# Performance work log

Hardware: AMD Instinct MI355X
Metric: run time of the kernel (lower is better)

The kernel has to match this reference:

```python
import jax, jax.numpy as jnp
import numpy as np

B, T, C = 4, 4096, 1024
NEG_INF = -1e38


def setup_inputs() -> dict:
    key = jax.random.key(0)
    ks = jax.random.split(key, 5)
    scale = 0.02  # realistic init scale for CxC projections
    x = jax.random.normal(ks[0], (B, T, C), dtype=jnp.float32)
    key_w = jax.random.normal(ks[1], (C, C), dtype=jnp.float32) * scale
    value_w = jax.random.normal(ks[2], (C, C), dtype=jnp.float32) * scale
    receptance_w = jax.random.normal(ks[3], (C, C), dtype=jnp.float32) * scale
    output_w = jax.random.normal(ks[4], (C, C), dtype=jnp.float32) * scale
    # deterministic param init matching the module's __init__
    time_decay = -5.0 + 8.0 * (jnp.arange(C, dtype=jnp.float32) / (C - 1)) ** 0.7
    time_first = jnp.full((C,), -3.0, dtype=jnp.float32)
    # initial WKV state as in forward() when state is None
    aa0 = jnp.zeros((B, C), dtype=jnp.float32)
    bb0 = jnp.zeros((B, C), dtype=jnp.float32)
    pp0 = jnp.full((B, C), NEG_INF, dtype=jnp.float32)
    return dict(x=x, key_w=key_w, value_w=value_w, receptance_w=receptance_w,
                output_w=output_w, time_decay=time_decay, time_first=time_first,
                aa0=aa0, bb0=bb0, pp0=pp0)


def reference(x, key_w, value_w, receptance_w, output_w,
              time_decay, time_first, aa0, bb0, pp0):
    # projections (torch Linear: y = x @ W.T)
    k = jnp.einsum('btc,dc->btd', x, key_w)        # [B,T,C]
    v = jnp.einsum('btc,dc->btd', x, value_w)      # [B,T,C]
    r = jax.nn.sigmoid(jnp.einsum('btc,dc->btd', x, receptance_w))
    w = jnp.exp(time_decay)  # [C]
    u = time_first           # [C]

    def step(carry, kv):
        aa, bb, pp = carry           # each [B,C]
        kt, vt = kv                  # each [B,C]
        # output at this step (numerically stabilized exp weighting)
        ww = u + kt
        p = jnp.maximum(pp, ww)
        e1 = jnp.exp(pp - p)
        e2 = jnp.exp(ww - p)
        wkv = (e1 * aa + e2 * vt) / (e1 * bb + e2)
        # state update
        ww2 = pp - w
        p2 = jnp.maximum(ww2, kt)
        e1b = jnp.exp(ww2 - p2)
        e2b = jnp.exp(kt - p2)
        return (e1b * aa + e2b * vt, e1b * bb + e2b, p2), wkv

    k_t = jnp.swapaxes(k, 0, 1)  # [T,B,C]
    v_t = jnp.swapaxes(v, 0, 1)
    (aa, bb, pp), wkv = jax.lax.scan(step, (aa0, bb0, pp0), (k_t, v_t))
    wkv = jnp.swapaxes(wkv, 0, 1)  # [B,T,C]

    out = jnp.einsum('btc,dc->btd', r * wkv, output_w)
    return out, aa, bb, pp
```

## Files before the change

kernel.cpp:

```cpp
#include <hip/hip_runtime.h>
#include <stdint.h>

#define BDIM 4
#define TDIM 4096
#define CDIM 1024
#define MDIM (BDIM * TDIM)
#define SSEG 64
#define LSEG 64
#define NCH  (BDIM * CDIM)

#define GK   1024
#define GK2  2048
#define NTK  16

typedef __attribute__((ext_vector_type(8))) short bf16x8;
typedef __attribute__((ext_vector_type(4))) float f32x4;

__device__ __forceinline__ unsigned short f2bf(float f) {
    unsigned u = __builtin_bit_cast(unsigned, f);
    u = u + 0x7fffu + ((u >> 16) & 1u);
    return (unsigned short)(u >> 16);
}
__device__ __forceinline__ float bf2f(unsigned short h) {
    unsigned u = ((unsigned)h) << 16;
    return __builtin_bit_cast(float, u);
}

typedef __attribute__((address_space(1))) const unsigned int g_u32;
typedef __attribute__((address_space(3))) unsigned int l_u32;
__device__ __forceinline__ void gload_lds16(const void* g, void* l) {
    __builtin_amdgcn_global_load_lds((g_u32*)g, (l_u32*)l, 16, 0, 0);
}

__global__ void castk(const float* __restrict__ src, unsigned short* __restrict__ dst, int n4) {
    int i = blockIdx.x * blockDim.x + threadIdx.x;
    int stride = gridDim.x * blockDim.x;
    for (int j = i; j < n4; j += stride) {
        float4 f = ((const float4*)src)[j];
        ushort4 o;
        o.x = f2bf(f.x); o.y = f2bf(f.y); o.z = f2bf(f.z); o.w = f2bf(f.w);
        ((ushort4*)dst)[j] = o;
    }
}

__global__ void castw(const float* __restrict__ kw, const float* __restrict__ vw,
                      const float* __restrict__ rw, const float* __restrict__ ow,
                      unsigned short* __restrict__ wf, unsigned short* __restrict__ owb) {
    int i = blockIdx.x * 256 + threadIdx.x;
    int m = i >> 18, j = i & 262143;
    const float* s = (m == 0) ? kw : (m == 1) ? vw : (m == 2) ? rw : ow;
    unsigned short* d = (m < 3) ? (wf + (size_t)m * 1048576) : owb;
    float4 f = ((const float4*)s)[j];
    ushort4 o;
    o.x = f2bf(f.x); o.y = f2bf(f.y); o.z = f2bf(f.z); o.w = f2bf(f.w);
    ((ushort4*)d)[j] = o;
}

template <int MODE, int NT>
__global__ __launch_bounds__(512, 2) void gemm256(
    const unsigned short* __restrict__ A,
    const unsigned short* __restrict__ Bw,
    unsigned short* __restrict__ oK, unsigned short* __restrict__ oV,
    unsigned short* __restrict__ oR, float* __restrict__ oF)
{
    extern __shared__ char sh[];
    char* shA = sh;
    char* shB = sh + 65536;

    const int tid  = threadIdx.x;
    const int wave = tid >> 6;
    const int lane = tid & 63;
    const int wm   = wave >> 2;
    const int wn   = wave & 3;
    const int lrow = lane & 15;
    const int koct = lane >> 4;

    const int kb0 = (koct * 16) ^ ((lrow & 7) << 4);
    const int kb1 = kb0 ^ 64;

    const int sr0  = tid >> 3;
    const int sc0  = ((tid & 7) * 16) ^ ((sr0 & 7) << 4);
    const int sr1  = (512 + tid) >> 3;
    const int sc1  = ((tid & 7) * 16) ^ ((sr1 & 7) << 4);
    const int sd0  = tid * 16;
    const int sd1  = 8192 + tid * 16;

    const int bid = blockIdx.x;
    const int xcd = bid & 7;
    const int idx = bid >> 3;
    const int mt  = xcd * 8 + idx / NT;
    const int nt  = idx % NT;
    const size_t row0 = (size_t)mt * 256;
    const size_t col0 = (size_t)nt * 256;

    const char* gA = (const char*)A  + row0 * GK2;
    const char* gB = (const char*)Bw + col0 * GK2;

    auto stage = [&](int tt, int part) {
        if (tt >= NTK) return;
        int slot = tt & 1;
        int isA  = (part < 2) ? 1 : 0;
        int half = part & 1;
        const char* gbase = (isA ? gA : gB) + (size_t)half * 128 * GK2 + tt * 128;
        char* lbase = (isA ? shA : shB) + (slot * 2 + half) * 16384;
        gload_lds16(gbase + (size_t)sr0 * GK2 + sc0, lbase + sd0);
        gload_lds16(gbase + (size_t)sr1 * GK2 + sc1, lbase + sd1);
    };

    stage(0, 0); stage(0, 1); stage(0, 2); stage(0, 3);
    stage(1, 0); stage(1, 1);
    asm volatile("s_waitcnt vmcnt(4)" ::: "memory");
    __builtin_amdgcn_s_barrier();

    f32x4 acc[8][4] = {};
    bf16x8 af[8][2], bf_[4][2];

    {
        const char* ab = shA + wm * 16384 + lrow * 128;
#pragma unroll
        for (int mi = 0; mi < 4; ++mi) {
            af[mi][0] = *(const bf16x8*)(ab + mi * 2048 + kb0);
            af[mi][1] = *(const bf16x8*)(ab + mi * 2048 + kb1);
        }
    }

    for (int t = 0; t < NTK; ++t) {
        const int slot  = t & 1;
        const char* ab  = shA + (slot * 2 + wm) * 16384 + lrow * 128;
        const char* bb  = shB + (slot * 2 + (wn >> 1)) * 16384 + ((wn & 1) * 64 + lrow) * 128;
        const char* abN = shA + (((t + 1) & 1) * 2 + wm) * 16384 + lrow * 128;

#pragma unroll
        for (int ni = 0; ni < 4; ++ni) {
            bf_[ni][0] = *(const bf16x8*)(bb + ni * 2048 + kb0);
            bf_[ni][1] = *(const bf16x8*)(bb + ni * 2048 + kb1);
        }
        stage(t + 1, 2);
        __builtin_amdgcn_s_barrier();
        __builtin_amdgcn_s_setprio(1);
#pragma unroll
        for (int a = 0; a < 4; ++a)
#pragma unroll
            for (int b = 0; b < 2; ++b)
#pragma unroll
                for (int ks = 0; ks < 2; ++ks)
                    acc[a][b] = __builtin_amdgcn_mfma_f32_16x16x32_bf16(af[a][ks], bf_[b][ks], acc[a][b], 0, 0, 0);
        __builtin_amdgcn_s_setprio(0);
        __builtin_amdgcn_s_barrier();

#pragma unroll
        for (int mi = 4; mi < 8; ++mi) {
            af[mi][0] = *(const bf16x8*)(ab + mi * 2048 + kb0);
            af[mi][1] = *(const bf16x8*)(ab + mi * 2048 + kb1);
        }
        stage(t + 1, 3);
        __builtin_amdgcn_s_barrier();
        __builtin_amdgcn_s_setprio(1);
#pragma unroll
        for (int a = 0; a < 4; ++a)
#pragma unroll
            for (int b = 0; b < 2; ++b)
#pragma unroll
                for (int ks = 0; ks < 2; ++ks)
                    acc[a][2 + b] = __builtin_amdgcn_mfma_f32_16x16x32_bf16(af[a][ks], bf_[2 + b][ks], acc[a][2 + b], 0, 0, 0);
        __builtin_amdgcn_s_setprio(0);
        __builtin_amdgcn_s_barrier();

        stage(t + 2, 0);
        __builtin_amdgcn_s_barrier();
        __builtin_amdgcn_s_setprio(1);
#pragma unroll
        for (int a = 0; a < 4; ++a)
#pragma unroll
            for (int b = 0; b < 2; ++b)
#pragma unroll
                for (int ks = 0; ks < 2; ++ks)
                    acc[4 + a][b] = __builtin_amdgcn_mfma_f32_16x16x32_bf16(af[4 + a][ks], bf_[b][ks], acc[4 + a][b], 0, 0, 0);
        __builtin_amdgcn_s_setprio(0);
        if (t <= 13)      asm volatile("s_waitcnt vmcnt(6)" ::: "memory");
        else if (t == 14) asm volatile("s_waitcnt vmcnt(4)" ::: "memory");
        __builtin_amdgcn_s_barrier();

        stage(t + 2, 1);
        if (t + 1 < NTK) {
#pragma unroll
            for (int mi = 0; mi < 4; ++mi) {
                af[mi][0] = *(const bf16x8*)(abN + mi * 2048 + kb0);
                af[mi][1] = *(const bf16x8*)(abN + mi * 2048 + kb1);
            }
        }
        __builtin_amdgcn_s_barrier();
        __builtin_amdgcn_s_setprio(1);
#pragma unroll
        for (int a = 0; a < 4; ++a)
#pragma unroll
            for (int b = 0; b < 2; ++b)
#pragma unroll
                for (int ks = 0; ks < 2; ++ks)
                    acc[4 + a][2 + b] = __builtin_amdgcn_mfma_f32_16x16x32_bf16(af[4 + a][ks], bf_[2 + b][ks], acc[4 + a][2 + b], 0, 0, 0);
        __builtin_amdgcn_s_setprio(0);
        if (t <= 13)      asm volatile("s_waitcnt vmcnt(4)" ::: "memory");
        else if (t == 14) asm volatile("s_waitcnt vmcnt(0)" ::: "memory");
        __builtin_amdgcn_s_barrier();
    }

    const int crow = (lane >> 4) * 4;
    const int ccol = lane & 15;
    if (MODE == 1) {
#pragma unroll
        for (int mi = 0; mi < 8; ++mi)
#pragma unroll
            for (int ni = 0; ni < 4; ++ni) {
                size_t gr = row0 + wm * 128 + mi * 16 + crow;
                size_t gc = col0 + wn * 64 + ni * 16 + ccol;
#pragma unroll
                for (int j = 0; j < 4; ++j)
                    oF[(gr + j) * 1024 + gc] = acc[mi][ni][j];
            }
    } else {
        const int region = nt >> 2;
        unsigned short* dst = (region == 0) ? oK : ((region == 1) ? oV : oR);
        const size_t cb0 = (size_t)(nt & 3) * 256;
#pragma unroll
        for (int mi = 0; mi < 8; ++mi)
#pragma unroll
            for (int ni = 0; ni < 4; ++ni) {
                size_t gr = row0 + wm * 128 + mi * 16 + crow;
                size_t gc = cb0 + wn * 64 + ni * 16 + ccol;
#pragma unroll
                for (int j = 0; j < 4; ++j) {
                    float val = acc[mi][ni][j];
                    if (region == 2) val = 1.0f / (1.0f + __expf(-val));
                    dst[(gr + j) * 1024 + gc] = f2bf(val);
                }
            }
    }
}

__global__ __launch_bounds__(256) void wkv_phase1(
    const unsigned short* __restrict__ kf, const unsigned short* __restrict__ vf,
    const float* __restrict__ td,
    float* __restrict__ segA, float* __restrict__ segB, float* __restrict__ segP)
{
    const int tid  = blockIdx.x * 256 + threadIdx.x;
    const int lane = tid & 63;
    const int wg   = tid >> 6;
    const int cg   = wg & 63;
    const int s    = wg >> 6;
    const int q    = cg * 64 + lane;
    const int b    = q >> 10;
    const int c    = q & (CDIM - 1);

    const float w = __expf(td[c]);

    float aa = 0.0f, bb = 0.0f, pp = -1e38f;
    size_t idx = (size_t)b * TDIM * CDIM + (size_t)(s * LSEG) * CDIM + c;
#pragma unroll 4
    for (int i = 0; i < LSEG; ++i, idx += CDIM) {
        float kt = bf2f(kf[idx]);
        float vt = bf2f(vf[idx]);
        float ww2 = pp - w;
        float p2  = fmaxf(ww2, kt);
        float e1  = __expf(ww2 - p2);
        float e2  = __expf(kt - p2);
        aa = e1 * aa + e2 * vt;
        bb = e1 * bb + e2;
        pp = p2;
    }
    segA[s * NCH + q] = aa;
    segB[s * NCH + q] = bb;
    segP[s * NCH + q] = pp;
}

__global__ __launch_bounds__(256) void wkv_phase2(
    const float* __restrict__ segA, const float* __restrict__ segB, const float* __restrict__ segP,
    const float* __restrict__ td,
    const float* __restrict__ aa0, const float* __restrict__ bb0, const float* __restrict__ pp0,
    float* __restrict__ preA, float* __restrict__ preB, float* __restrict__ preP,
    float* __restrict__ stout)
{
    const int tid = blockIdx.x * 256 + threadIdx.x;
    const int c = tid & (CDIM - 1);
    const float w  = __expf(td[c]);
    const float Lw = (float)LSEG * w;

    float aa = aa0[tid], bb = bb0[tid], pp = pp0[tid];
    for (int s = 0; s < SSEG; ++s) {
        preA[s * NCH + tid] = aa;
        preB[s * NCH + tid] = bb;
        preP[s * NCH + tid] = pp;
        float al = segA[s * NCH + tid];
        float bl = segB[s * NCH + tid];
        float pl = segP[s * NCH + tid];
        float ppd = pp - Lw;
        float p  = fmaxf(ppd, pl);
        float e1 = __expf(ppd - p);
        float e2 = __expf(pl - p);
        aa = e1 * aa + e2 * al;
        bb = e1 * bb + e2 * bl;
        pp = p;
    }
    stout[tid]           = aa;
    stout[NCH + tid]     = bb;
    stout[2 * NCH + tid] = pp;
}

__global__ __launch_bounds__(256) void wkv_phase3(
    const unsigned short* __restrict__ kf, const unsigned short* __restrict__ vf,
    const unsigned short* __restrict__ rb,
    const float* __restrict__ td, const float* __restrict__ tf,
    const float* __restrict__ preA, const float* __restrict__ preB, const float* __restrict__ preP,
    unsigned short* __restrict__ rwkvb)
{
    const int tid  = blockIdx.x * 256 + threadIdx.x;
    const int lane = tid & 63;
    const int wg   = tid >> 6;
    const int cg   = wg & 63;
    const int s    = wg >> 6;
    const int q    = cg * 64 + lane;
    const int b    = q >> 10;
    const int c    = q & (CDIM - 1);

    const float w = __expf(td[c]);
    const float u = tf[c];

    float aa = preA[s * NCH + q];
    float bb = preB[s * NCH + q];
    float pp = preP[s * NCH + q];

    size_t idx = (size_t)b * TDIM * CDIM + (size_t)(s * LSEG) * CDIM + c;
#pragma unroll 4
    for (int i = 0; i < LSEG; ++i, idx += CDIM) {
        float kt = bf2f(kf[idx]);
        float vt = bf2f(vf[idx]);
        float rt = bf2f(rb[idx]);
        float ww = u + kt;
        float p  = fmaxf(pp, ww);
        float e1 = __expf(pp - p);
        float e2 = __expf(ww - p);
        float wkv = (e1 * aa + e2 * vt) / (e1 * bb + e2);
        rwkvb[idx] = f2bf(rt * wkv);
        float ww2 = pp - w;
        float p2  = fmaxf(ww2, kt);
        float e1b = __expf(ww2 - p2);
        float e2b = __expf(kt - p2);
        aa = e1b * aa + e2b * vt;
        bb = e1b * bb + e2b;
        pp = p2;
    }
}

extern "C" void kernel_launch(void* const* d_in, const int* in_sizes, int n_in,
                              void* d_out, int out_size, void* d_ws, size_t ws_size,
                              hipStream_t stream) {
    const float* x   = (const float*)d_in[0];
    const float* kw  = (const float*)d_in[1];
    const float* vw  = (const float*)d_in[2];
    const float* rw  = (const float*)d_in[3];
    const float* ow  = (const float*)d_in[4];
    const float* td  = (const float*)d_in[5];
    const float* tf  = (const float*)d_in[6];
    const float* aa0 = (const float*)d_in[7];
    const float* bb0 = (const float*)d_in[8];
    const float* pp0 = (const float*)d_in[9];
    float* out = (float*)d_out;

    char* ws = (char*)d_ws;
    unsigned short* wf    = (unsigned short*)(ws);
    unsigned short* owb   = (unsigned short*)(ws + 6291456);
    unsigned short* xb    = (unsigned short*)(ws + 8388608);
    unsigned short* kfb   = (unsigned short*)(ws + 41943040);
    unsigned short* vfb   = (unsigned short*)(ws + 75497472);
    unsigned short* rbb   = (unsigned short*)(ws + 109051904);
    unsigned short* rwkvb = (unsigned short*)(ws + 142606336);
    float* segA = (float*)(ws + 176160768);
    float* segB = (float*)(ws + 177209344);
    float* segP = (float*)(ws + 178257920);
    float* preA = (float*)(ws + 179306496);
    float* preB = (float*)(ws + 180355072);
    float* preP = (float*)(ws + 181403648);

    hipFuncSetAttribute((const void*)(gemm256<0, 12>), hipFuncAttributeMaxDynamicSharedMemorySize, 131072);
    hipFuncSetAttribute((const void*)(gemm256<1, 4>),  hipFuncAttributeMaxDynamicSharedMemorySize, 131072);

    castk<<<2048, 256, 0, stream>>>(x, xb, MDIM * CDIM / 4);
    castw<<<4096, 256, 0, stream>>>(kw, vw, rw, ow, wf, owb);

    gemm256<0, 12><<<768, 512, 131072, stream>>>(xb, wf, kfb, vfb, rbb, nullptr);

    wkv_phase1<<<NCH * SSEG / 256, 256, 0, stream>>>(kfb, vfb, td, segA, segB, segP);
    wkv_phase2<<<NCH / 256, 256, 0, stream>>>(segA, segB, segP, td, aa0, bb0, pp0,
                                              preA, preB, preP, out + (size_t)MDIM * CDIM);
    wkv_phase3<<<NCH * SSEG / 256, 256, 0, stream>>>(kfb, vfb, rbb, td, tf,
                                                     preA, preB, preP, rwkvb);

    gemm256<1, 4><<<256, 512, 131072, stream>>>(rwkvb, owb, nullptr, nullptr, nullptr, out);
}
```

Baseline: 223.0 us.

## Loop each GEMM block over K/V/R projections instead of launching 768 blocks

The fused KVR projection GEMM now launches 256 blocks, and each block loops over the three weight matrices (NP=3) for the same A row-tile. Before, 768 blocks each handled one 256x256 output tile. The intent is to cut the grid to one wave of blocks on 256 CUs, avoiding a partial tail wave, and to improve L2 reuse of the A tile across the three projections. The trade-off is that each block runs three times longer serially, and all A tiles are reloaded from global memory on every pass, so latency hiding across blocks is reduced.

```diff
diff --git a/kernel.cpp b/kernel.cpp
--- a/kernel.cpp
+++ b/kernel.cpp
@@ -56,7 +56,7 @@
     ((ushort4*)d)[j] = o;
 }
 
-template <int MODE, int NT>
+template <int MODE, int NT, int NP>
 __global__ __launch_bounds__(512, 2) void gemm256(
     const unsigned short* __restrict__ A,
     const unsigned short* __restrict__ Bw,
@@ -91,149 +91,152 @@
     const int mt  = xcd * 8 + idx / NT;
     const int nt  = idx % NT;
     const size_t row0 = (size_t)mt * 256;
-    const size_t col0 = (size_t)nt * 256;
-
-    const char* gA = (const char*)A  + row0 * GK2;
-    const char* gB = (const char*)Bw + col0 * GK2;
-
-    auto stage = [&](int tt, int part) {
-        if (tt >= NTK) return;
-        int slot = tt & 1;
-        int isA  = (part < 2) ? 1 : 0;
-        int half = part & 1;
-        const char* gbase = (isA ? gA : gB) + (size_t)half * 128 * GK2 + tt * 128;
-        char* lbase = (isA ? shA : shB) + (slot * 2 + half) * 16384;
-        gload_lds16(gbase + (size_t)sr0 * GK2 + sc0, lbase + sd0);
-        gload_lds16(gbase + (size_t)sr1 * GK2 + sc1, lbase + sd1);
-    };
-
-    stage(0, 0); stage(0, 1); stage(0, 2); stage(0, 3);
-    stage(1, 0); stage(1, 1);
-    asm volatile("s_waitcnt vmcnt(4)" ::: "memory");
-    __builtin_amdgcn_s_barrier();
-
-    f32x4 acc[8][4] = {};
-    bf16x8 af[8][2], bf_[4][2];
-
-    {
-        const char* ab = shA + wm * 16384 + lrow * 128;
-#pragma unroll
-        for (int mi = 0; mi < 4; ++mi) {
-            af[mi][0] = *(const bf16x8*)(ab + mi * 2048 + kb0);
-            af[mi][1] = *(const bf16x8*)(ab + mi * 2048 + kb1);
-        }
-    }
-
-    for (int t = 0; t < NTK; ++t) {
-        const int slot  = t & 1;
-        const char* ab  = shA + (slot * 2 + wm) * 16384 + lrow * 128;
-        const char* bb  = shB + (slot * 2 + (wn >> 1)) * 16384 + ((wn & 1) * 64 + lrow) * 128;
-        const char* abN = shA + (((t + 1) & 1) * 2 + wm) * 16384 + lrow * 128;
-
-#pragma unroll
-        for (int ni = 0; ni < 4; ++ni) {
-            bf_[ni][0] = *(const bf16x8*)(bb + ni * 2048 + kb0);
-            bf_[ni][1] = *(const bf16x8*)(bb + ni * 2048 + kb1);
-        }
-        stage(t + 1, 2);
+    const size_t colb = (size_t)nt * 256;
+
+    const char* gA = (const char*)A + row0 * GK2;
+
+    for (int p = 0; p < NP; ++p) {
+        const char* gB = (const char*)Bw + ((size_t)p * 1024 + colb) * GK2;
+
+        auto stage = [&](int tt, int part) {
+            if (tt >= NTK) return;
+            int slot = tt & 1;
+            int isA  = (part < 2) ? 1 : 0;
+            int half = part & 1;
+            const char* gbase = (isA ? gA : gB) + (size_t)half * 128 * GK2 + tt * 128;
+            char* lbase = (isA ? shA : shB) + (slot * 2 + half) * 16384;
+            gload_lds16(gbase + (size_t)sr0 * GK2 + sc0, lbase + sd0);
+            gload_lds16(gbase + (size_t)sr1 * GK2 + sc1, lbase + sd1);
+        };
+
         __builtin_amdgcn_s_barrier();
-        __builtin_amdgcn_s_setprio(1);
-#pragma unroll
-        for (int a = 0; a < 4; ++a)
-#pragma unroll
-            for (int b = 0; b < 2; ++b)
-#pragma unroll
-                for (int ks = 0; ks < 2; ++ks)
-                    acc[a][b] = __builtin_amdgcn_mfma_f32_16x16x32_bf16(af[a][ks], bf_[b][ks], acc[a][b], 0, 0, 0);
-        __builtin_amdgcn_s_setprio(0);
+
+        stage(0, 0); stage(0, 1); stage(0, 2); stage(0, 3);
+        stage(1, 0); stage(1, 1);
+        asm volatile("s_waitcnt vmcnt(4)" ::: "memory");
         __builtin_amdgcn_s_barrier();
 
-#pragma unroll
-        for (int mi = 4; mi < 8; ++mi) {
-            af[mi][0] = *(const bf16x8*)(ab + mi * 2048 + kb0);
-            af[mi][1] = *(const bf16x8*)(ab + mi * 2048 + kb1);
-        }
-        stage(t + 1, 3);
-        __builtin_amdgcn_s_barrier();
-        __builtin_amdgcn_s_setprio(1);
-#pragma unroll
-        for (int a = 0; a < 4; ++a)
-#pragma unroll
-            for (int b = 0; b < 2; ++b)
-#pragma unroll
-                for (int ks = 0; ks < 2; ++ks)
-                    acc[a][2 + b] = __builtin_amdgcn_mfma_f32_16x16x32_bf16(af[a][ks], bf_[2 + b][ks], acc[a][2 + b], 0, 0, 0);
-        __builtin_amdgcn_s_setprio(0);
-        __builtin_amdgcn_s_barrier();
-
-        stage(t + 2, 0);
-        __builtin_amdgcn_s_barrier();
-        __builtin_amdgcn_s_setprio(1);
-#pragma unroll
-        for (int a = 0; a < 4; ++a)
-#pragma unroll
-            for (int b = 0; b < 2; ++b)
-#pragma unroll
-                for (int ks = 0; ks < 2; ++ks)
-                    acc[4 + a][b] = __builtin_amdgcn_mfma_f32_16x16x32_bf16(af[4 + a][ks], bf_[b][ks], acc[4 + a][b], 0, 0, 0);
-        __builtin_amdgcn_s_setprio(0);
-        if (t <= 13)      asm volatile("s_waitcnt vmcnt(6)" ::: "memory");
-        else if (t == 14) asm volatile("s_waitcnt vmcnt(4)" ::: "memory");
-        __builtin_amdgcn_s_barrier();
-
-        stage(t + 2, 1);
-        if (t + 1 < NTK) {
+        f32x4 acc[8][4] = {};
+        bf16x8 af[8][2], bf_[4][2];
+
+        {
+            const char* ab0 = shA + wm * 16384 + lrow * 128;
 #pragma unroll
             for (int mi = 0; mi < 4; ++mi) {
-                af[mi][0] = *(const bf16x8*)(abN + mi * 2048 + kb0);
-                af[mi][1] = *(const bf16x8*)(abN + mi * 2048 + kb1);
+                af[mi][0] = *(const bf16x8*)(ab0 + mi * 2048 + kb0);
+                af[mi][1] = *(const bf16x8*)(ab0 + mi * 2048 + kb1);
             }
         }
-        __builtin_amdgcn_s_barrier();
-        __builtin_amdgcn_s_setprio(1);
-#pragma unroll
-        for (int a = 0; a < 4; ++a)
-#pragma unroll
-            for (int b = 0; b < 2; ++b)
-#pragma unroll
-                for (int ks = 0; ks < 2; ++ks)
-                    acc[4 + a][2 + b] = __builtin_amdgcn_mfma_f32_16x16x32_bf16(af[4 + a][ks], bf_[2 + b][ks], acc[4 + a][2 + b], 0, 0, 0);
-        __builtin_amdgcn_s_setprio(0);
-        if (t <= 13)      asm volatile("s_waitcnt vmcnt(4)" ::: "memory");
-        else if (t == 14) asm volatile("s_waitcnt vmcnt(0)" ::: "memory");
-        __builtin_amdgcn_s_barrier();
-    }
-
-    const int crow = (lane >> 4) * 4;
-    const int ccol = lane & 15;
-    if (MODE == 1) {
-#pragma unroll
-        for (int mi = 0; mi < 8; ++mi)
+
+        for (int t = 0; t < NTK; ++t) {
+            const int slot  = t & 1;
+            const char* ab  = shA + (slot * 2 + wm) * 16384 + lrow * 128;
+            const char* bb  = shB + (slot * 2 + (wn >> 1)) * 16384 + ((wn & 1) * 64 + lrow) * 128;
+            const char* abN = shA + (((t + 1) & 1) * 2 + wm) * 16384 + lrow * 128;
+
 #pragma unroll
             for (int ni = 0; ni < 4; ++ni) {
-                size_t gr = row0 + wm * 128 + mi * 16 + crow;
-                size_t gc = col0 + wn * 64 + ni * 16 + ccol;
-#pragma unroll
-                for (int j = 0; j < 4; ++j)
-                    oF[(gr + j) * 1024 + gc] = acc[mi][ni][j];
+                bf_[ni][0] = *(const bf16x8*)(bb + ni * 2048 + kb0);
+                bf_[ni][1] = *(const bf16x8*)(bb + ni * 2048 + kb1);
             }
-    } else {
-        const int region = nt >> 2;
-        unsigned short* dst = (region == 0) ? oK : ((region == 1) ? oV : oR);
-        const size_t cb0 = (size_t)(nt & 3) * 256;
-#pragma unroll
-        for (int mi = 0; mi < 8; ++mi)
-#pragma unroll
-            for (int ni = 0; ni < 4; ++ni) {
-                size_t gr = row0 + wm * 128 + mi * 16 + crow;
-                size_t gc = cb0 + wn * 64 + ni * 16 + ccol;
-#pragma unroll
-                for (int j = 0; j < 4; ++j) {
-                    float val = acc[mi][ni][j];
-                    if (region == 2) val = 1.0f / (1.0f + __expf(-val));
-                    dst[(gr + j) * 1024 + gc] = f2bf(val);
+            stage(t + 1, 2);
+            __builtin_amdgcn_s_barrier();
+            __builtin_amdgcn_s_setprio(1);
+#pragma unroll
+            for (int a = 0; a < 4; ++a)
+#pragma unroll
+                for (int b = 0; b < 2; ++b)
+#pragma unroll
+                    for (int ks = 0; ks < 2; ++ks)
+                        acc[a][b] = __builtin_amdgcn_mfma_f32_16x16x32_bf16(af[a][ks], bf_[b][ks], acc[a][b], 0, 0, 0);
+            __builtin_amdgcn_s_setprio(0);
+            __builtin_amdgcn_s_barrier();
+
+#pragma unroll
+            for (int mi = 4; mi < 8; ++mi) {
+                af[mi][0] = *(const bf16x8*)(ab + mi * 2048 + kb0);
+                af[mi][1] = *(const bf16x8*)(ab + mi * 2048 + kb1);
+            }
+            stage(t + 1, 3);
+            __builtin_amdgcn_s_barrier();
+            __builtin_amdgcn_s_setprio(1);
+#pragma unroll
+            for (int a = 0; a < 4; ++a)
+#pragma unroll
+                for (int b = 0; b < 2; ++b)
+#pragma unroll
+                    for (int ks = 0; ks < 2; ++ks)
+                        acc[a][2 + b] = __builtin_amdgcn_mfma_f32_16x16x32_bf16(af[a][ks], bf_[2 + b][ks], acc[a][2 + b], 0, 0, 0);
+            __builtin_amdgcn_s_setprio(0);
+            __builtin_amdgcn_s_barrier();
+
+            stage(t + 2, 0);
+            __builtin_amdgcn_s_barrier();
+            __builtin_amdgcn_s_setprio(1);
+#pragma unroll
+            for (int a = 0; a < 4; ++a)
+#pragma unroll
+                for (int b = 0; b < 2; ++b)
+#pragma unroll
+                    for (int ks = 0; ks < 2; ++ks)
+                        acc[4 + a][b] = __builtin_amdgcn_mfma_f32_16x16x32_bf16(af[4 + a][ks], bf_[b][ks], acc[4 + a][b], 0, 0, 0);
+            __builtin_amdgcn_s_setprio(0);
+            if (t <= 13)      asm volatile("s_waitcnt vmcnt(6)" ::: "memory");
+            else if (t == 14) asm volatile("s_waitcnt vmcnt(4)" ::: "memory");
+            __builtin_amdgcn_s_barrier();
+
+            stage(t + 2, 1);
+            if (t + 1 < NTK) {
+#pragma unroll
+                for (int mi = 0; mi < 4; ++mi) {
+                    af[mi][0] = *(const bf16x8*)(abN + mi * 2048 + kb0);
+                    af[mi][1] = *(const bf16x8*)(abN + mi * 2048 + kb1);
                 }
             }
+            __builtin_amdgcn_s_barrier();
+            __builtin_amdgcn_s_setprio(1);
+#pragma unroll
+            for (int a = 0; a < 4; ++a)
+#pragma unroll
+                for (int b = 0; b < 2; ++b)
+#pragma unroll
+                    for (int ks = 0; ks < 2; ++ks)
+                        acc[4 + a][2 + b] = __builtin_amdgcn_mfma_f32_16x16x32_bf16(af[4 + a][ks], bf_[2 + b][ks], acc[4 + a][2 + b], 0, 0, 0);
+            __builtin_amdgcn_s_setprio(0);
+            if (t <= 13)      asm volatile("s_waitcnt vmcnt(4)" ::: "memory");
+            else if (t == 14) asm volatile("s_waitcnt vmcnt(0)" ::: "memory");
+            __builtin_amdgcn_s_barrier();
+        }
+
+        const int crow = (lane >> 4) * 4;
+        const int ccol = lane & 15;
+        if (MODE == 1) {
+#pragma unroll
+            for (int mi = 0; mi < 8; ++mi)
+#pragma unroll
+                for (int ni = 0; ni < 4; ++ni) {
+                    size_t gr = row0 + wm * 128 + mi * 16 + crow;
+                    size_t gc = colb + wn * 64 + ni * 16 + ccol;
+#pragma unroll
+                    for (int j = 0; j < 4; ++j)
+                        oF[(gr + j) * 1024 + gc] = acc[mi][ni][j];
+                }
+        } else {
+            unsigned short* dst = (p == 0) ? oK : ((p == 1) ? oV : oR);
+#pragma unroll
+            for (int mi = 0; mi < 8; ++mi)
+#pragma unroll
+                for (int ni = 0; ni < 4; ++ni) {
+                    size_t gr = row0 + wm * 128 + mi * 16 + crow;
+                    size_t gc = colb + wn * 64 + ni * 16 + ccol;
+#pragma unroll
+                    for (int j = 0; j < 4; ++j) {
+                        float val = acc[mi][ni][j];
+                        if (p == 2) val = 1.0f / (1.0f + __expf(-val));
+                        dst[(gr + j) * 1024 + gc] = f2bf(val);
+                    }
+                }
+        }
     }
 }
 
@@ -380,13 +383,13 @@
     float* preB = (float*)(ws + 180355072);
     float* preP = (float*)(ws + 181403648);
 
-    hipFuncSetAttribute((const void*)(gemm256<0, 12>), hipFuncAttributeMaxDynamicSharedMemorySize, 131072);
-    hipFuncSetAttribute((const void*)(gemm256<1, 4>),  hipFuncAttributeMaxDynamicSharedMemorySize, 131072);
+    hipFuncSetAttribute((const void*)(gemm256<0, 4, 3>), hipFuncAttributeMaxDynamicSharedMemorySize, 131072);
+    hipFuncSetAttribute((const void*)(gemm256<1, 4, 1>), hipFuncAttributeMaxDynamicSharedMemorySize, 131072);
 
     castk<<<2048, 256, 0, stream>>>(x, xb, MDIM * CDIM / 4);
     castw<<<4096, 256, 0, stream>>>(kw, vw, rw, ow, wf, owb);
 
-    gemm256<0, 12><<<768, 512, 131072, stream>>>(xb, wf, kfb, vfb, rbb, nullptr);
+    gemm256<0, 4, 3><<<256, 512, 131072, stream>>>(xb, wf, kfb, vfb, rbb, nullptr);
 
     wkv_phase1<<<NCH * SSEG / 256, 256, 0, stream>>>(kfb, vfb, td, segA, segB, segP);
     wkv_phase2<<<NCH / 256, 256, 0, stream>>>(segA, segB, segP, td, aa0, bb0, pp0,
@@ -394,5 +397,5 @@
     wkv_phase3<<<NCH * SSEG / 256, 256, 0, stream>>>(kfb, vfb, rbb, td, tf,
                                                      preA, preB, preP, rwkvb);
 
-    gemm256<1, 4><<<256, 512, 131072, stream>>>(rwkvb, owb, nullptr, nullptr, nullptr, out);
-}
+    gemm256<1, 4, 1><<<256, 512, 131072, stream>>>(rwkvb, owb, nullptr, nullptr, nullptr, out);
+}
```

New measurement: 250.0 us. 12.1% more time.

## Merge cast kernels and restructure GEMM main loop into two phases

Applied to the files above, without the earlier changes.

Combines the activation and weight fp32-to-bf16 casts into one launch, removing a kernel launch and the grid-stride loop. The GEMM inner loop goes from four barrier-separated MFMA quarters to two halves, each issuing two staging loads before a larger MFMA block. This cuts barriers per K step and gives bigger MFMA bursts, but changes the vmcnt wait scheme and the load/compute interleave, which risks exposing memory latency or introducing a race on the LDS slots.

```diff
diff --git a/kernel.cpp b/kernel.cpp
--- a/kernel.cpp
+++ b/kernel.cpp
@@ -32,24 +32,23 @@
     __builtin_amdgcn_global_load_lds((g_u32*)g, (l_u32*)l, 16, 0, 0);
 }
 
-__global__ void castk(const float* __restrict__ src, unsigned short* __restrict__ dst, int n4) {
-    int i = blockIdx.x * blockDim.x + threadIdx.x;
-    int stride = gridDim.x * blockDim.x;
-    for (int j = i; j < n4; j += stride) {
-        float4 f = ((const float4*)src)[j];
-        ushort4 o;
-        o.x = f2bf(f.x); o.y = f2bf(f.y); o.z = f2bf(f.z); o.w = f2bf(f.w);
-        ((ushort4*)dst)[j] = o;
-    }
-}
-
-__global__ void castw(const float* __restrict__ kw, const float* __restrict__ vw,
-                      const float* __restrict__ rw, const float* __restrict__ ow,
-                      unsigned short* __restrict__ wf, unsigned short* __restrict__ owb) {
+__global__ void castall(const float* __restrict__ x,
+                        const float* __restrict__ kw, const float* __restrict__ vw,
+                        const float* __restrict__ rw, const float* __restrict__ ow,
+                        unsigned short* __restrict__ xb,
+                        unsigned short* __restrict__ wf, unsigned short* __restrict__ owb) {
     int i = blockIdx.x * 256 + threadIdx.x;
-    int m = i >> 18, j = i & 262143;
-    const float* s = (m == 0) ? kw : (m == 1) ? vw : (m == 2) ? rw : ow;
-    unsigned short* d = (m < 3) ? (wf + (size_t)m * 1048576) : owb;
+    const float* s;
+    unsigned short* d;
+    int j;
+    if (i < 4194304) {
+        s = x; d = xb; j = i;
+    } else {
+        int k = i - 4194304;
+        int m = k >> 18; j = k & 262143;
+        s = (m == 0) ? kw : (m == 1) ? vw : (m == 2) ? rw : ow;
+        d = (m < 3) ? (wf + (size_t)m * 1048576) : owb;
+    }
     float4 f = ((const float4*)s)[j];
     ushort4 o;
     o.x = f2bf(f.x); o.y = f2bf(f.y); o.z = f2bf(f.z); o.w = f2bf(f.w);
@@ -116,11 +115,11 @@
     bf16x8 af[8][2], bf_[4][2];
 
     {
-        const char* ab = shA + wm * 16384 + lrow * 128;
+        const char* ab0 = shA + wm * 16384 + lrow * 128;
 #pragma unroll
         for (int mi = 0; mi < 4; ++mi) {
-            af[mi][0] = *(const bf16x8*)(ab + mi * 2048 + kb0);
-            af[mi][1] = *(const bf16x8*)(ab + mi * 2048 + kb1);
+            af[mi][0] = *(const bf16x8*)(ab0 + mi * 2048 + kb0);
+            af[mi][1] = *(const bf16x8*)(ab0 + mi * 2048 + kb1);
         }
     }
 
@@ -135,53 +134,26 @@
             bf_[ni][0] = *(const bf16x8*)(bb + ni * 2048 + kb0);
             bf_[ni][1] = *(const bf16x8*)(bb + ni * 2048 + kb1);
         }
-        stage(t + 1, 2);
-        __builtin_amdgcn_s_barrier();
-        __builtin_amdgcn_s_setprio(1);
-#pragma unroll
-        for (int a = 0; a < 4; ++a)
-#pragma unroll
-            for (int b = 0; b < 2; ++b)
-#pragma unroll
-                for (int ks = 0; ks < 2; ++ks)
-                    acc[a][b] = __builtin_amdgcn_mfma_f32_16x16x32_bf16(af[a][ks], bf_[b][ks], acc[a][b], 0, 0, 0);
-        __builtin_amdgcn_s_setprio(0);
-        __builtin_amdgcn_s_barrier();
-
 #pragma unroll
         for (int mi = 4; mi < 8; ++mi) {
             af[mi][0] = *(const bf16x8*)(ab + mi * 2048 + kb0);
             af[mi][1] = *(const bf16x8*)(ab + mi * 2048 + kb1);
         }
+        stage(t + 1, 2);
         stage(t + 1, 3);
         __builtin_amdgcn_s_barrier();
         __builtin_amdgcn_s_setprio(1);
 #pragma unroll
         for (int a = 0; a < 4; ++a)
 #pragma unroll
-            for (int b = 0; b < 2; ++b)
+            for (int b = 0; b < 4; ++b)
 #pragma unroll
                 for (int ks = 0; ks < 2; ++ks)
-                    acc[a][2 + b] = __builtin_amdgcn_mfma_f32_16x16x32_bf16(af[a][ks], bf_[2 + b][ks], acc[a][2 + b], 0, 0, 0);
+                    acc[a][b] = __builtin_amdgcn_mfma_f32_16x16x32_bf16(af[a][ks], bf_[b][ks], acc[a][b], 0, 0, 0);
         __builtin_amdgcn_s_setprio(0);
+        if (t <= 14)      asm volatile("s_waitcnt vmcnt(4)" ::: "memory");
         __builtin_amdgcn_s_barrier();
 
-        stage(t + 2, 0);
-        __builtin_amdgcn_s_barrier();
-        __builtin_amdgcn_s_setprio(1);
-#pragma unroll
-        for (int a = 0; a < 4; ++a)
-#pragma unroll
-            for (int b = 0; b < 2; ++b)
-#pragma unroll
-                for (int ks = 0; ks < 2; ++ks)
-                    acc[4 + a][b] = __builtin_amdgcn_mfma_f32_16x16x32_bf16(af[4 + a][ks], bf_[b][ks], acc[4 + a][b], 0, 0, 0);
-        __builtin_amdgcn_s_setprio(0);
-        if (t <= 13)      asm volatile("s_waitcnt vmcnt(6)" ::: "memory");
-        else if (t == 14) asm volatile("s_waitcnt vmcnt(4)" ::: "memory");
-        __builtin_amdgcn_s_barrier();
-
-        stage(t + 2, 1);
         if (t + 1 < NTK) {
 #pragma unroll
             for (int mi = 0; mi < 4; ++mi) {
@@ -189,15 +161,17 @@
                 af[mi][1] = *(const bf16x8*)(abN + mi * 2048 + kb1);
             }
         }
+        stage(t + 2, 0);
+        stage(t + 2, 1);
         __builtin_amdgcn_s_barrier();
         __builtin_amdgcn_s_setprio(1);
 #pragma unroll
         for (int a = 0; a < 4; ++a)
 #pragma unroll
-            for (int b = 0; b < 2; ++b)
+            for (int b = 0; b < 4; ++b)
 #pragma unroll
                 for (int ks = 0; ks < 2; ++ks)
-                    acc[4 + a][2 + b] = __builtin_amdgcn_mfma_f32_16x16x32_bf16(af[4 + a][ks], bf_[2 + b][ks], acc[4 + a][2 + b], 0, 0, 0);
+                    acc[4 + a][b] = __builtin_amdgcn_mfma_f32_16x16x32_bf16(af[4 + a][ks], bf_[b][ks], acc[4 + a][b], 0, 0, 0);
         __builtin_amdgcn_s_setprio(0);
         if (t <= 13)      asm volatile("s_waitcnt vmcnt(4)" ::: "memory");
         else if (t == 14) asm volatile("s_waitcnt vmcnt(0)" ::: "memory");
@@ -383,8 +357,7 @@
     hipFuncSetAttribute((const void*)(gemm256<0, 12>), hipFuncAttributeMaxDynamicSharedMemorySize, 131072);
     hipFuncSetAttribute((const void*)(gemm256<1, 4>),  hipFuncAttributeMaxDynamicSharedMemorySize, 131072);
 
-    castk<<<2048, 256, 0, stream>>>(x, xb, MDIM * CDIM / 4);
-    castw<<<4096, 256, 0, stream>>>(kw, vw, rw, ow, wf, owb);
+    castall<<<20480, 256, 0, stream>>>(x, kw, vw, rw, ow, xb, wf, owb);
 
     gemm256<0, 12><<<768, 512, 131072, stream>>>(xb, wf, kfb, vfb, rbb, nullptr);
 
```

Result: no change. 219.5 us, median of 2 (-1.6%).
